# Kernel optimization log

Hardware: AMD Instinct MI355X
Metric: run time of the kernel (lower is better)

## Reference

```python
import jax, jax.numpy as jnp
import numpy as np
from functools import partial

V, CTX, D, H, L, FF = 50257, 1024, 768, 12, 12, 3072
DH = D // H
EPS = 1e-5


def _ln(x, g, b):
    m = jnp.mean(x, axis=-1, keepdims=True)
    v = jnp.mean(jnp.square(x - m), axis=-1, keepdims=True)
    return (x - m) * jax.lax.rsqrt(v + EPS) * g + b


def setup_inputs() -> dict:
    key = jax.random.key(0)
    ks = jax.random.split(key, 8)
    s = 0.02
    return {
        "input_ids": jax.random.randint(ks[0], (2, 1024), 0, V),
        "token_emb": jax.random.normal(ks[1], (V, D), jnp.float32) * s,
        "pos_emb": jax.random.normal(ks[2], (CTX, D), jnp.float32) * s,
        "ln1_g": jnp.ones((L, D), jnp.float32),
        "ln1_b": jnp.zeros((L, D), jnp.float32),
        "qkv_w": jax.random.normal(ks[3], (L, 3 * D, D), jnp.float32) * s,
        "out_w": jax.random.normal(ks[4], (L, D, D), jnp.float32) * (s / np.sqrt(2 * L)),
        "ln2_g": jnp.ones((L, D), jnp.float32),
        "ln2_b": jnp.zeros((L, D), jnp.float32),
        "ff1_w": jax.random.normal(ks[5], (L, FF, D), jnp.float32) * s,
        "ff2_w": jax.random.normal(ks[6], (L, D, FF), jnp.float32) * s,
        "lnf_g": jnp.ones((D,), jnp.float32),
        "lnf_b": jnp.zeros((D,), jnp.float32),
    }


def reference(input_ids, token_emb, pos_emb, ln1_g, ln1_b, qkv_w, out_w,
              ln2_g, ln2_b, ff1_w, ff2_w, lnf_g, lnf_b):
    B, T = input_ids.shape
    x = token_emb[input_ids] + pos_emb[:T]  # [B,T,D]
    causal = jnp.tril(jnp.ones((T, T), bool))  # True = keep
    scale = 1.0 / np.sqrt(DH)

    def block(x, p):
        g1, b1, wqkv, wo, g2, b2, w1, w2 = p
        h = _ln(x, g1, b1)
        qkv = h @ wqkv.T  # [B,T,3D]
        q, k, v = jnp.split(qkv, 3, axis=-1)
        q = q.reshape(B, T, H, DH).transpose(0, 2, 1, 3)
        k = k.reshape(B, T, H, DH).transpose(0, 2, 1, 3)
        v = v.reshape(B, T, H, DH).transpose(0, 2, 1, 3)
        scores = jnp.einsum('bhqd,bhkd->bhqk', q, k) * scale
        scores = jnp.where(causal, scores, -jnp.inf)
        w = jax.nn.softmax(scores, axis=-1)
        o = jnp.einsum('bhqk,bhkd->bhqd', w, v)
        o = o.transpose(0, 2, 1, 3).reshape(B, T, D) @ wo.T
        x = x + o
        h2 = _ln(x, g2, b2)
        ff = jax.nn.gelu(h2 @ w1.T, approximate=False) @ w2.T
        return x + ff, None

    params = (ln1_g, ln1_b, qkv_w, out_w, ln2_g, ln2_b, ff1_w, ff2_w)
    x, _ = jax.lax.scan(block, x, params)
    x = _ln(x, lnf_g, lnf_b)
    logits = x @ token_emb.T  # tied lm head
    return logits
```

## Files before the change

### kernel.cpp

```cpp
#include <hip/hip_runtime.h>
#include <hip/hip_bf16.h>
#include <math.h>

#define D_MODEL 768
#define NHEAD 12
#define DHEAD 64
#define NLAYER 12
#define FF_DIM 3072
#define SEQ 1024
#define TOKENS 2048
#define VOCAB 50257

typedef short bf16x8 __attribute__((ext_vector_type(8)));
typedef float f32x4 __attribute__((ext_vector_type(4)));
typedef unsigned short u16x4 __attribute__((ext_vector_type(4)));
typedef unsigned short u16x8 __attribute__((ext_vector_type(8)));

__device__ inline unsigned short f2bf(float f) {
    union { float f; unsigned u; } un;
    un.f = f;
    unsigned u = un.u;
    u += 0x7fffu + ((u >> 16) & 1u);
    return (unsigned short)(u >> 16);
}

__device__ inline void gl_lds16(const void* g, void* l) {
    __builtin_amdgcn_global_load_lds(
        (const __attribute__((address_space(1))) unsigned int*)g,
        (__attribute__((address_space(3))) unsigned int*)l, 16, 0, 0);
}

template<int N> __device__ __forceinline__ void waitcnt_vm() {
    static_assert(N == 0 || N == 3 || N == 4 || N == 5 || N == 6 || N == 8, "add case");
    if constexpr (N == 0) asm volatile("s_waitcnt vmcnt(0)" ::: "memory");
    else if constexpr (N == 3) asm volatile("s_waitcnt vmcnt(3)" ::: "memory");
    else if constexpr (N == 4) asm volatile("s_waitcnt vmcnt(4)" ::: "memory");
    else if constexpr (N == 5) asm volatile("s_waitcnt vmcnt(5)" ::: "memory");
    else if constexpr (N == 6) asm volatile("s_waitcnt vmcnt(6)" ::: "memory");
    else if constexpr (N == 8) asm volatile("s_waitcnt vmcnt(8)" ::: "memory");
}

__global__ __launch_bounds__(256) void cvt_kernel(const float* __restrict__ s,
                                                  unsigned short* __restrict__ d,
                                                  long n4) {
    long i = (long)blockIdx.x * 256 + threadIdx.x;
    long stride = (long)gridDim.x * 256;
    for (; i < n4; i += stride) {
        f32x4 v = ((const f32x4*)s)[i];
        u16x4 r;
        r[0] = f2bf(v[0]); r[1] = f2bf(v[1]); r[2] = f2bf(v[2]); r[3] = f2bf(v[3]);
        ((u16x4*)d)[i] = r;
    }
}

__global__ __launch_bounds__(256) void embed_kernel(const int* __restrict__ ids,
                                                    const float* __restrict__ tok,
                                                    const float* __restrict__ pos,
                                                    float* __restrict__ x) {
    int i = blockIdx.x * 256 + threadIdx.x;
    int row = i / D_MODEL;
    int d = i - row * D_MODEL;
    int t = row & (SEQ - 1);
    x[i] = tok[(long)ids[row] * D_MODEL + d] + pos[(long)t * D_MODEL + d];
}

__global__ __launch_bounds__(256) void ln_kernel(const float* __restrict__ x,
                                                 const float* __restrict__ g,
                                                 const float* __restrict__ b,
                                                 unsigned short* __restrict__ out) {
    int row = blockIdx.x;
    int tid = threadIdx.x;
    const float* xr = x + (long)row * D_MODEL;
    float v0 = xr[tid], v1 = xr[tid + 256], v2 = xr[tid + 512];
    __shared__ float sm[4];
    float s = v0 + v1 + v2;
    #pragma unroll
    for (int off = 32; off; off >>= 1) s += __shfl_xor(s, off);
    if ((tid & 63) == 0) sm[tid >> 6] = s;
    __syncthreads();
    float mean = (sm[0] + sm[1] + sm[2] + sm[3]) * (1.f / D_MODEL);
    __syncthreads();
    float d0 = v0 - mean, d1 = v1 - mean, d2 = v2 - mean;
    s = d0 * d0 + d1 * d1 + d2 * d2;
    #pragma unroll
    for (int off = 32; off; off >>= 1) s += __shfl_xor(s, off);
    if ((tid & 63) == 0) sm[tid >> 6] = s;
    __syncthreads();
    float var = (sm[0] + sm[1] + sm[2] + sm[3]) * (1.f / D_MODEL);
    float rs = rsqrtf(var + 1e-5f);
    unsigned short* orow = out + (long)row * D_MODEL;
    orow[tid]       = f2bf(d0 * rs * g[tid]       + b[tid]);
    orow[tid + 256] = f2bf(d1 * rs * g[tid + 256] + b[tid + 256]);
    orow[tid + 512] = f2bf(d2 * rs * g[tid + 512] + b[tid + 512]);
}

#define GM_NONE 0
#define GM_RES  1
#define GM_GELU 2
#define GM_QKV  3

template<int WM, int WN, int MODE, int DB>
__global__ __launch_bounds__(256) void gemm_bf16(
        const unsigned short* __restrict__ A, const unsigned short* __restrict__ W,
        int M, int N, int K,
        float* __restrict__ Cf, unsigned short* __restrict__ Cb,
        const float* __restrict__ RES,
        unsigned short* __restrict__ P1, unsigned short* __restrict__ P2) {
    constexpr int BM = WM * 32, BN = WN * 32;
    constexpr int NLD = BM / 32 + BN / 32;
    __shared__ unsigned short lA[DB][BM * 64];
    __shared__ unsigned short lB[DB][BN * 64];

    int tid = threadIdx.x;
    int lane = tid & 63, wv = tid >> 6;
    int wr = wv >> 1, wc = wv & 1;
    int lr = lane & 15, kq = lane >> 4;
    int row0 = blockIdx.x * BM;
    int col0 = blockIdx.y * BN;

    int srow_in = tid >> 3;
    int ssp = tid & 7;
    int skg = ssp ^ (srow_in & 7);
    int lbase = ((tid & ~63)) << 3;

    f32x4 acc[WM][WN];
    #pragma unroll
    for (int m = 0; m < WM; m++)
        #pragma unroll
        for (int n = 0; n < WN; n++) acc[m][n] = (f32x4){0.f, 0.f, 0.f, 0.f};

    auto stage = [&](int buf, int kt) {
        #pragma unroll
        for (int i = 0; i < BM / 32; i++) {
            int row = i * 32 + srow_in;
            gl_lds16(A + (size_t)(row0 + row) * K + kt + skg * 8,
                     &lA[buf][i * 2048 + lbase]);
        }
        #pragma unroll
        for (int i = 0; i < BN / 32; i++) {
            int row = i * 32 + srow_in;
            int srow = col0 + row;
            if (srow >= N) srow = N - 1;
            gl_lds16(W + (size_t)srow * K + kt + skg * 8,
                     &lB[buf][i * 2048 + lbase]);
        }
    };
    auto compute = [&](int buf) {
        #pragma unroll
        for (int kk = 0; kk < 2; kk++) {
            int kg = kk * 4 + kq;
            bf16x8 af[WM], bfr[WN];
            #pragma unroll
            for (int m = 0; m < WM; m++) {
                int row = wr * (WM * 16) + m * 16 + lr;
                af[m] = *(const bf16x8*)&lA[buf][row * 64 + ((kg ^ (row & 7)) << 3)];
            }
            #pragma unroll
            for (int n = 0; n < WN; n++) {
                int row = wc * (WN * 16) + n * 16 + lr;
                bfr[n] = *(const bf16x8*)&lB[buf][row * 64 + ((kg ^ (row & 7)) << 3)];
            }
            #pragma unroll
            for (int m = 0; m < WM; m++)
                #pragma unroll
                for (int n = 0; n < WN; n++)
                    acc[m][n] = __builtin_amdgcn_mfma_f32_16x16x32_bf16(af[m], bfr[n], acc[m][n], 0, 0, 0);
        }
    };

    if (DB == 2) {
        stage(0, 0);
        __builtin_amdgcn_sched_barrier(0);
        int nt = K >> 6;
        int cur = 0;
        for (int t = 0; t < nt; t++) {
            if (t + 1 < nt) {
                stage(cur ^ 1, (t + 1) << 6);
                __builtin_amdgcn_sched_barrier(0);
                waitcnt_vm<NLD>();
            } else {
                waitcnt_vm<0>();
            }
            __builtin_amdgcn_s_barrier();
            __builtin_amdgcn_sched_barrier(0);
            compute(cur);
            __builtin_amdgcn_sched_barrier(0);
            __builtin_amdgcn_s_barrier();
            cur ^= 1;
        }
    } else {
        for (int kt = 0; kt < K; kt += 64) {
            stage(0, kt);
            __syncthreads();
            compute(0);
            __syncthreads();
        }
    }

    #pragma unroll
    for (int m = 0; m < WM; m++) {
        int r0 = row0 + wr * (WM * 16) + m * 16 + (kq << 2);
        #pragma unroll
        for (int n = 0; n < WN; n++) {
            int c = col0 + wc * (WN * 16) + n * 16 + lr;
            if (c < N) {
                if (MODE == GM_QKV) {
                    int bb = r0 >> 10, t0q = r0 & 1023;
                    if (c < D_MODEL) {
                        int h = c >> 6, dh = c & 63;
                        size_t base = (((size_t)(bb * NHEAD + h) * SEQ) + t0q) * 64 + dh;
                        #pragma unroll
                        for (int j = 0; j < 4; j++)
                            P1[base + (size_t)j * 64] = f2bf(acc[m][n][j] * 0.125f);
                    } else if (c < 2 * D_MODEL) {
                        int cc = c - D_MODEL;
                        int h = cc >> 6, dh = cc & 63;
                        size_t base = (((size_t)(bb * NHEAD + h) * SEQ) + t0q) * 64 + dh;
                        #pragma unroll
                        for (int j = 0; j < 4; j++)
                            P2[base + (size_t)j * 64] = f2bf(acc[m][n][j]);
                    } else {
                        int cc = c - 2 * D_MODEL;
                        int h = cc >> 6, dh = cc & 63;
                        u16x4 vv;
                        #pragma unroll
                        for (int j = 0; j < 4; j++) vv[j] = f2bf(acc[m][n][j]);
                        *(u16x4*)(Cb + ((size_t)(bb * NHEAD + h) * 64 + dh) * SEQ + t0q) = vv;
                    }
                } else {
                    #pragma unroll
                    for (int j = 0; j < 4; j++) {
                        int r = r0 + j;
                        size_t idx = (size_t)r * N + c;
                        float v = acc[m][n][j];
                        if (MODE == GM_RES) {
                            Cf[idx] = v + RES[idx];
                        } else if (MODE == GM_GELU) {
                            Cb[idx] = f2bf(0.5f * v * (1.f + erff(v * 0.70710678118f)));
                        } else {
                            Cf[idx] = v;
                        }
                    }
                }
            }
        }
    }
}

#define ANW 4
__global__ __launch_bounds__(256) void attn_mfma(const unsigned short* __restrict__ Qb,
                                                 const unsigned short* __restrict__ Kb,
                                                 const unsigned short* __restrict__ Vt,
                                                 unsigned short* __restrict__ att) {
    int b = blockIdx.z, h = blockIdx.y, pr = blockIdx.x;
    int tid = threadIdx.x, l = tid & 63, w = tid >> 6;
    int lr = l & 15, hg = l >> 4;
    int hk8 = hg * 8, hg4 = hg * 4;
    size_t bh = (size_t)b * NHEAD + h;
    const unsigned short* Qp = Qb + bh * SEQ * 64;
    const unsigned short* Kp = Kb + bh * SEQ * 64;
    const unsigned short* Vp = Vt + bh * 64 * SEQ;

    __shared__ float sm_m[ANW][2][16], sm_l[ANW][2][16];
    __shared__ float sm_o[ANW][2][16][65];
    __shared__ unsigned short pl[ANW][1024];
    unsigned short* Pw = &pl[w][0];

    #pragma unroll
    for (int ti = 0; ti < 2; ti++) {
        int tile = ti ? (63 - pr) : pr;
        int q0 = tile * 16;
        bf16x8 qf0 = *(const bf16x8*)(Qp + (size_t)(q0 + lr) * 64 + hk8);
        bf16x8 qf1 = *(const bf16x8*)(Qp + (size_t)(q0 + lr) * 64 + 32 + hk8);
        f32x4 O[4];
        #pragma unroll
        for (int dt = 0; dt < 4; dt++) O[dt] = (f32x4){0.f, 0.f, 0.f, 0.f};
        f32x4 mrun = (f32x4){-1e30f, -1e30f, -1e30f, -1e30f};
        f32x4 lrun = (f32x4){0.f, 0.f, 0.f, 0.f};
        int nch = (tile >> 2) + 1;

        bf16x8 kfa[8];
        if (w < nch) {
            int k0p = w * 64;
            #pragma unroll
            for (int kt = 0; kt < 4; kt++) {
                kfa[2 * kt]     = *(const bf16x8*)(Kp + (size_t)(k0p + kt * 16 + lr) * 64 + hk8);
                kfa[2 * kt + 1] = *(const bf16x8*)(Kp + (size_t)(k0p + kt * 16 + lr) * 64 + 32 + hk8);
            }
        }

        for (int c = w; c < nch; c += ANW) {
            int k0 = c * 64;
            f32x4 S[4];
            #pragma unroll
            for (int kt = 0; kt < 4; kt++) {
                S[kt] = (f32x4){0.f, 0.f, 0.f, 0.f};
                S[kt] = __builtin_amdgcn_mfma_f32_16x16x32_bf16(qf0, kfa[2 * kt], S[kt], 0, 0, 0);
                S[kt] = __builtin_amdgcn_mfma_f32_16x16x32_bf16(qf1, kfa[2 * kt + 1], S[kt], 0, 0, 0);
            }
            bf16x8 kfb[8];
            int cn = c + ANW;
            if (cn < nch) {
                int k0n = cn * 64;
                #pragma unroll
                for (int kt = 0; kt < 4; kt++) {
                    kfb[2 * kt]     = *(const bf16x8*)(Kp + (size_t)(k0n + kt * 16 + lr) * 64 + hk8);
                    kfb[2 * kt + 1] = *(const bf16x8*)(Kp + (size_t)(k0n + kt * 16 + lr) * 64 + 32 + hk8);
                }
            }
            if (c == nch - 1) {
                #pragma unroll
                for (int kt = 0; kt < 4; kt++)
                    #pragma unroll
                    for (int j = 0; j < 4; j++)
                        S[kt][j] = (k0 + kt * 16 + lr <= q0 + hg4 + j) ? S[kt][j] : -3.0e38f;
            }
            f32x4 rm;
            #pragma unroll
            for (int j = 0; j < 4; j++)
                rm[j] = fmaxf(fmaxf(S[0][j], S[1][j]), fmaxf(S[2][j], S[3][j]));
            #pragma unroll
            for (int msk = 1; msk <= 8; msk <<= 1)
                #pragma unroll
                for (int j = 0; j < 4; j++)
                    rm[j] = fmaxf(rm[j], __shfl_xor(rm[j], msk));
            f32x4 mn, corr, rs;
            #pragma unroll
            for (int j = 0; j < 4; j++) {
                mn[j] = fmaxf(mrun[j], rm[j]);
                corr[j] = __expf(mrun[j] - mn[j]);
                rs[j] = 0.f;
            }
            #pragma unroll
            for (int kt = 0; kt < 4; kt++)
                #pragma unroll
                for (int j = 0; j < 4; j++) {
                    float p = __expf(S[kt][j] - mn[j]);
                    S[kt][j] = p;
                    rs[j] += p;
                }
            #pragma unroll
            for (int msk = 1; msk <= 8; msk <<= 1)
                #pragma unroll
                for (int j = 0; j < 4; j++)
                    rs[j] += __shfl_xor(rs[j], msk);
            #pragma unroll
            for (int j = 0; j < 4; j++) {
                lrun[j] = lrun[j] * corr[j] + rs[j];
                mrun[j] = mn[j];
            }
            #pragma unroll
            for (int dt = 0; dt < 4; dt++)
                #pragma unroll
                for (int j = 0; j < 4; j++) O[dt][j] *= corr[j];
            bf16x8 vfr[8];
            #pragma unroll
            for (int dt = 0; dt < 4; dt++) {
                vfr[2 * dt]     = *(const bf16x8*)(Vp + (size_t)(dt * 16 + lr) * SEQ + k0 + hk8);
                vfr[2 * dt + 1] = *(const bf16x8*)(Vp + (size_t)(dt * 16 + lr) * SEQ + k0 + 32 + hk8);
            }
            #pragma unroll
            for (int kt = 0; kt < 4; kt++) {
                int cc = kt * 16 + lr;
                int slot = cc >> 3, off = cc & 7;
                #pragma unroll
                for (int j = 0; j < 4; j++) {
                    int r = hg4 + j;
                    Pw[r * 64 + ((slot ^ (r & 7)) << 3) + off] = f2bf(S[kt][j]);
                }
            }
            asm volatile("s_waitcnt lgkmcnt(0)" ::: "memory");
            bf16x8 pf0 = *(const bf16x8*)&Pw[lr * 64 + ((hg ^ (lr & 7)) << 3)];
            bf16x8 pf1 = *(const bf16x8*)&Pw[lr * 64 + (((4 + hg) ^ (lr & 7)) << 3)];
            #pragma unroll
            for (int dt = 0; dt < 4; dt++) {
                O[dt] = __builtin_amdgcn_mfma_f32_16x16x32_bf16(pf0, vfr[2 * dt], O[dt], 0, 0, 0);
                O[dt] = __builtin_amdgcn_mfma_f32_16x16x32_bf16(pf1, vfr[2 * dt + 1], O[dt], 0, 0, 0);
            }
            #pragma unroll
            for (int i = 0; i < 8; i++) kfa[i] = kfb[i];
        }
        if (lr == 0) {
            #pragma unroll
            for (int j = 0; j < 4; j++) {
                sm_m[w][ti][hg4 + j] = mrun[j];
                sm_l[w][ti][hg4 + j] = lrun[j];
            }
        }
        #pragma unroll
        for (int dt = 0; dt < 4; dt++)
            #pragma unroll
            for (int j = 0; j < 4; j++)
                sm_o[w][ti][hg4 + j][dt * 16 + lr] = O[dt][j];
    }
    __syncthreads();
    {
        int ti2 = w >> 1;
        int tile = ti2 ? (63 - pr) : pr;
        int q0 = tile * 16;
        #pragma unroll
        for (int jj = 0; jj < 2; jj++) {
            int j = (w & 1) * 2 + jj;
            int r = hg4 + j;
            float m0 = sm_m[0][ti2][r], m1 = sm_m[1][ti2][r];
            float m2 = sm_m[2][ti2][r], m3 = sm_m[3][ti2][r];
            float M = fmaxf(fmaxf(m0, m1), fmaxf(m2, m3));
            float e0 = __expf(m0 - M), e1 = __expf(m1 - M);
            float e2 = __expf(m2 - M), e3 = __expf(m3 - M);
            float L = sm_l[0][ti2][r] * e0 + sm_l[1][ti2][r] * e1
                    + sm_l[2][ti2][r] * e2 + sm_l[3][ti2][r] * e3;
            float invL = 1.f / L;
            unsigned short* orow = att + ((size_t)(b * SEQ + q0 + r)) * D_MODEL + h * 64;
            #pragma unroll
            for (int dt = 0; dt < 4; dt++) {
                int cidx = dt * 16 + lr;
                float o = sm_o[0][ti2][r][cidx] * e0 + sm_o[1][ti2][r][cidx] * e1
                        + sm_o[2][ti2][r][cidx] * e2 + sm_o[3][ti2][r][cidx] * e3;
                orow[cidx] = f2bf(o * invL);
            }
        }
    }
}

extern "C" void kernel_launch(void* const* d_in, const int* in_sizes, int n_in,
                              void* d_out, int out_size, void* d_ws, size_t ws_size,
                              hipStream_t stream) {
    const int*   input_ids = (const int*)d_in[0];
    const float* token_emb = (const float*)d_in[1];
    const float* pos_emb   = (const float*)d_in[2];
    const float* ln1_g     = (const float*)d_in[3];
    const float* ln1_b     = (const float*)d_in[4];
    const float* qkv_w     = (const float*)d_in[5];
    const float* out_w     = (const float*)d_in[6];
    const float* ln2_g     = (const float*)d_in[7];
    const float* ln2_b     = (const float*)d_in[8];
    const float* ff1_w     = (const float*)d_in[9];
    const float* ff2_w     = (const float*)d_in[10];
    const float* lnf_g     = (const float*)d_in[11];
    const float* lnf_b     = (const float*)d_in[12];
    float* out = (float*)d_out;

    const size_t SZ_QKV_L = (size_t)3 * D_MODEL * D_MODEL;
    const size_t SZ_OUT_L = (size_t)D_MODEL * D_MODEL;
    const size_t SZ_FF1_L = (size_t)FF_DIM * D_MODEL;
    const size_t SZ_FF2_L = (size_t)D_MODEL * FF_DIM;
    const size_t SZ_TOK   = (size_t)VOCAB * D_MODEL;

    char* base = (char*)d_ws;
    size_t off = 0;
    auto alloc = [&](size_t bytes) -> char* {
        char* p = base + off;
        off = (off + bytes + 255) & ~(size_t)255;
        return p;
    };

    float* x              = (float*)alloc((size_t)TOKENS * D_MODEL * 4);
    unsigned short* hb    = (unsigned short*)alloc((size_t)TOKENS * D_MODEL * 2);
    unsigned short* attb  = (unsigned short*)alloc((size_t)TOKENS * D_MODEL * 2);
    unsigned short* ffab  = (unsigned short*)alloc((size_t)TOKENS * FF_DIM * 2);
    unsigned short* Qb    = (unsigned short*)alloc((size_t)TOKENS * D_MODEL * 2);
    unsigned short* Kb    = (unsigned short*)alloc((size_t)TOKENS * D_MODEL * 2);
    unsigned short* Vtb   = (unsigned short*)alloc((size_t)TOKENS * D_MODEL * 2);

    size_t act_end = off;
    size_t full_need = act_end + 2 * (NLAYER * (SZ_QKV_L + SZ_OUT_L + SZ_FF1_L + SZ_FF2_L) + SZ_TOK)
                       + 6 * 256;
    bool full = ws_size >= full_need;

    unsigned short *qkvA, *outA, *ff1A, *ff2A, *tokA;
    if (full) {
        qkvA = (unsigned short*)alloc(2 * NLAYER * SZ_QKV_L);
        outA = (unsigned short*)alloc(2 * NLAYER * SZ_OUT_L);
        ff1A = (unsigned short*)alloc(2 * NLAYER * SZ_FF1_L);
        ff2A = (unsigned short*)alloc(2 * NLAYER * SZ_FF2_L);
        tokA = (unsigned short*)alloc(2 * SZ_TOK);
    } else {
        qkvA = (unsigned short*)alloc(2 * SZ_QKV_L);
        outA = (unsigned short*)alloc(2 * SZ_OUT_L);
        ff1A = (unsigned short*)alloc(2 * SZ_FF1_L);
        ff2A = (unsigned short*)alloc(2 * SZ_FF2_L);
        tokA = (unsigned short*)alloc(2 * SZ_TOK);
    }

    auto cvt = [&](const float* s, unsigned short* d, size_t n) {
        long n4 = (long)(n / 4);
        int g = (int)((n4 + 255) / 256);
        if (g > 2048) g = 2048;
        cvt_kernel<<<g, 256, 0, stream>>>(s, d, n4);
    };

    if (full) {
        cvt(qkv_w, qkvA, NLAYER * SZ_QKV_L);
        cvt(out_w, outA, NLAYER * SZ_OUT_L);
        cvt(ff1_w, ff1A, NLAYER * SZ_FF1_L);
        cvt(ff2_w, ff2A, NLAYER * SZ_FF2_L);
        cvt(token_emb, tokA, SZ_TOK);
    }

    embed_kernel<<<TOKENS * D_MODEL / 256, 256, 0, stream>>>(input_ids, token_emb, pos_emb, x);

    for (int l = 0; l < NLAYER; l++) {
        const unsigned short* qw = full ? qkvA + (size_t)l * SZ_QKV_L : qkvA;
        const unsigned short* ow = full ? outA + (size_t)l * SZ_OUT_L : outA;
        const unsigned short* f1 = full ? ff1A + (size_t)l * SZ_FF1_L : ff1A;
        const unsigned short* f2 = full ? ff2A + (size_t)l * SZ_FF2_L : ff2A;

        ln_kernel<<<TOKENS, 256, 0, stream>>>(x, ln1_g + l * D_MODEL, ln1_b + l * D_MODEL, hb);
        if (!full) cvt(qkv_w + (size_t)l * SZ_QKV_L, qkvA, SZ_QKV_L);
        gemm_bf16<2, 3, GM_QKV, 2><<<dim3(TOKENS / 64, 3 * D_MODEL / 96), 256, 0, stream>>>(
            hb, qw, TOKENS, 3 * D_MODEL, D_MODEL, nullptr, Vtb, nullptr, Qb, Kb);
        attn_mfma<<<dim3(32, NHEAD, 2), 256, 0, stream>>>(Qb, Kb, Vtb, attb);
        if (!full) cvt(out_w + (size_t)l * SZ_OUT_L, outA, SZ_OUT_L);
        gemm_bf16<1, 2, GM_RES, 2><<<dim3(TOKENS / 32, D_MODEL / 64), 256, 0, stream>>>(
            attb, ow, TOKENS, D_MODEL, D_MODEL, x, nullptr, x, nullptr, nullptr);
        ln_kernel<<<TOKENS, 256, 0, stream>>>(x, ln2_g + l * D_MODEL, ln2_b + l * D_MODEL, hb);
        if (!full) cvt(ff1_w + (size_t)l * SZ_FF1_L, ff1A, SZ_FF1_L);
        gemm_bf16<2, 3, GM_GELU, 2><<<dim3(TOKENS / 64, FF_DIM / 96), 256, 0, stream>>>(
            hb, f1, TOKENS, FF_DIM, D_MODEL, nullptr, ffab, nullptr, nullptr, nullptr);
        if (!full) cvt(ff2_w + (size_t)l * SZ_FF2_L, ff2A, SZ_FF2_L);
        gemm_bf16<1, 2, GM_RES, 2><<<dim3(TOKENS / 32, D_MODEL / 64), 256, 0, stream>>>(
            ffab, f2, TOKENS, D_MODEL, FF_DIM, x, nullptr, x, nullptr, nullptr);
    }

    ln_kernel<<<TOKENS, 256, 0, stream>>>(x, lnf_g, lnf_b, hb);
    if (!full) cvt(token_emb, tokA, SZ_TOK);
    gemm_bf16<4, 4, GM_NONE, 2><<<dim3(TOKENS / 128, (VOCAB + 127) / 128), 256, 0, stream>>>(
        hb, tokA, TOKENS, VOCAB, D_MODEL, out, nullptr, nullptr, nullptr, nullptr);
}
```

Measured before the change: 1.998 ms.

## Add 256x256-tile GEMM kernel for LM head and widen FF1 tile

Adds a dedicated LM-head GEMM that uses 256x256 output tiles, 512 threads, double-buffered XOR-swizzled LDS staging and 8x4 MFMA accumulators per wave. The goal is more operand reuse per loaded byte on the large vocab projection. The FF1 GEMM also moves to a wider 2x4 wave tile with 128-column blocks. The large tile needs 128KB of LDS and many accumulator registers, which may limit occupancy. It also wastes work on the ragged last vocab tile.

```diff
diff --git a/kernel.cpp b/kernel.cpp
--- a/kernel.cpp
+++ b/kernel.cpp
@@ -247,6 +247,103 @@
     }
 }
 
+__global__ __launch_bounds__(512, 2) void gemm256_bf16(
+        const unsigned short* __restrict__ A, const unsigned short* __restrict__ W,
+        int M, int N, int K, float* __restrict__ Cf) {
+    __shared__ unsigned short lA[2][256 * 64];
+    __shared__ unsigned short lB[2][256 * 64];
+
+    int tid = threadIdx.x;
+    int lane = tid & 63, wv = tid >> 6;
+    int wr = wv >> 2, wc = wv & 3;
+    int lr = lane & 15, kq = lane >> 4;
+    int row0 = blockIdx.x * 256;
+    int col0 = blockIdx.y * 256;
+
+    int srow_in = tid >> 3;
+    int skg = (tid & 7) ^ (srow_in & 7);
+    int lbase = (tid & ~63) << 3;
+
+    f32x4 acc[8][4];
+    #pragma unroll
+    for (int m = 0; m < 8; m++)
+        #pragma unroll
+        for (int n = 0; n < 4; n++) acc[m][n] = (f32x4){0.f, 0.f, 0.f, 0.f};
+
+    auto stage = [&](int buf, int kt) {
+        #pragma unroll
+        for (int i = 0; i < 4; i++) {
+            int row = i * 64 + srow_in;
+            gl_lds16(A + (size_t)(row0 + row) * K + kt + skg * 8,
+                     &lA[buf][i * 4096 + lbase]);
+        }
+        #pragma unroll
+        for (int i = 0; i < 4; i++) {
+            int row = i * 64 + srow_in;
+            int srow = col0 + row;
+            if (srow >= N) srow = N - 1;
+            gl_lds16(W + (size_t)srow * K + kt + skg * 8,
+                     &lB[buf][i * 4096 + lbase]);
+        }
+    };
+    auto compute = [&](int buf) {
+        #pragma unroll
+        for (int kk = 0; kk < 2; kk++) {
+            int kg = kk * 4 + kq;
+            bf16x8 af[8], bfr[4];
+            #pragma unroll
+            for (int m = 0; m < 8; m++) {
+                int row = wr * 128 + m * 16 + lr;
+                af[m] = *(const bf16x8*)&lA[buf][row * 64 + ((kg ^ (row & 7)) << 3)];
+            }
+            #pragma unroll
+            for (int n = 0; n < 4; n++) {
+                int row = wc * 64 + n * 16 + lr;
+                bfr[n] = *(const bf16x8*)&lB[buf][row * 64 + ((kg ^ (row & 7)) << 3)];
+            }
+            #pragma unroll
+            for (int m = 0; m < 8; m++)
+                #pragma unroll
+                for (int n = 0; n < 4; n++)
+                    acc[m][n] = __builtin_amdgcn_mfma_f32_16x16x32_bf16(af[m], bfr[n], acc[m][n], 0, 0, 0);
+        }
+    };
+
+    stage(0, 0);
+    __builtin_amdgcn_sched_barrier(0);
+    int nt = K >> 6;
+    int cur = 0;
+    for (int t = 0; t < nt; t++) {
+        if (t + 1 < nt) {
+            stage(cur ^ 1, (t + 1) << 6);
+            __builtin_amdgcn_sched_barrier(0);
+            waitcnt_vm<8>();
+        } else {
+            waitcnt_vm<0>();
+        }
+        __builtin_amdgcn_s_barrier();
+        __builtin_amdgcn_sched_barrier(0);
+        compute(cur);
+        __builtin_amdgcn_sched_barrier(0);
+        __builtin_amdgcn_s_barrier();
+        cur ^= 1;
+    }
+
+    #pragma unroll
+    for (int m = 0; m < 8; m++) {
+        int r0 = row0 + wr * 128 + m * 16 + (kq << 2);
+        #pragma unroll
+        for (int n = 0; n < 4; n++) {
+            int c = col0 + wc * 64 + n * 16 + lr;
+            if (c < N) {
+                #pragma unroll
+                for (int j = 0; j < 4; j++)
+                    Cf[(size_t)(r0 + j) * N + c] = acc[m][n][j];
+            }
+        }
+    }
+}
+
 #define ANW 4
 __global__ __launch_bounds__(256) void attn_mfma(const unsigned short* __restrict__ Qb,
                                                  const unsigned short* __restrict__ Kb,
@@ -515,7 +612,7 @@
             attb, ow, TOKENS, D_MODEL, D_MODEL, x, nullptr, x, nullptr, nullptr);
         ln_kernel<<<TOKENS, 256, 0, stream>>>(x, ln2_g + l * D_MODEL, ln2_b + l * D_MODEL, hb);
         if (!full) cvt(ff1_w + (size_t)l * SZ_FF1_L, ff1A, SZ_FF1_L);
-        gemm_bf16<2, 3, GM_GELU, 2><<<dim3(TOKENS / 64, FF_DIM / 96), 256, 0, stream>>>(
+        gemm_bf16<2, 4, GM_GELU, 2><<<dim3(TOKENS / 64, FF_DIM / 128), 256, 0, stream>>>(
             hb, f1, TOKENS, FF_DIM, D_MODEL, nullptr, ffab, nullptr, nullptr, nullptr);
         if (!full) cvt(ff2_w + (size_t)l * SZ_FF2_L, ff2A, SZ_FF2_L);
         gemm_bf16<1, 2, GM_RES, 2><<<dim3(TOKENS / 32, D_MODEL / 64), 256, 0, stream>>>(
@@ -524,6 +621,6 @@
 
     ln_kernel<<<TOKENS, 256, 0, stream>>>(x, lnf_g, lnf_b, hb);
     if (!full) cvt(token_emb, tokA, SZ_TOK);
-    gemm_bf16<4, 4, GM_NONE, 2><<<dim3(TOKENS / 128, (VOCAB + 127) / 128), 256, 0, stream>>>(
-        hb, tokA, TOKENS, VOCAB, D_MODEL, out, nullptr, nullptr, nullptr, nullptr);
-}
+    gemm256_bf16<<<dim3(TOKENS / 256, (VOCAB + 255) / 256), 512, 0, stream>>>(
+        hb, tokA, TOKENS, VOCAB, D_MODEL, out);
+}
```

Result: no change. 1.987 ms, median of 2 (-0.6%).
